# Kernel tuning notes

Hardware: AMD Instinct MI355X
Metric: run time of the kernel (lower is better)

## Reference

```python
import jax, jax.numpy as jnp
import numpy as np

NUM_EMBEDDINGS = 1024
EMBEDDING_DIM = 64


def setup_inputs() -> dict:
    key = jax.random.key(0)
    k1, k2 = jax.random.split(key)
    x = jax.random.normal(k1, (32, 64, 32, 32), dtype=jnp.float32)
    # embeddings initialized uniform(-1/K, 1/K) as in the torch module
    codebook = jax.random.uniform(
        k2, (NUM_EMBEDDINGS, EMBEDDING_DIM), dtype=jnp.float32,
        minval=-1.0 / NUM_EMBEDDINGS, maxval=1.0 / NUM_EMBEDDINGS)
    return {"x": x, "codebook": codebook}


def reference(x, codebook):
    # x: [B, D, H, W] -> [B, H, W, D]
    xp = jnp.transpose(x, (0, 2, 3, 1))
    B, H, W, D = xp.shape
    K = codebook.shape[0]
    xf = xp.reshape(-1, D)  # [N, D]
    # squared L2 distances via expansion (argmin identical to torch.norm argmin)
    x2 = jnp.sum(xf * xf, axis=1, keepdims=True)          # [N, 1]
    c2 = jnp.sum(codebook * codebook, axis=1)             # [K]
    d2 = x2 - 2.0 * (xf @ codebook.T) + c2[None, :]       # [N, K]
    idx = jnp.argmin(d2, axis=1)                          # [N]
    encodings = jax.nn.one_hot(idx, K, dtype=jnp.float32)  # [N, K]
    quantized = codebook[idx]                             # [N, D] == encodings @ codebook
    quantized = quantized.reshape(B, H, W, D).transpose(0, 3, 1, 2)
    return encodings, quantized
```

## Files before the change

### kernel.cpp

```cpp
#include <hip/hip_runtime.h>

#define N_PIX   32768
#define DIM     64
#define K_CODES 1024
#define NCHUNK  8
#define CHUNK   (K_CODES / NCHUNK)


__global__ __launch_bounds__(256) void c2_kernel(const float* __restrict__ cb,
                                                 float* __restrict__ c2) {
    int k = blockIdx.x * 256 + threadIdx.x;
    if (k >= K_CODES) return;
    const float* row = cb + k * DIM;
    float a0 = 0.f, a1 = 0.f, a2 = 0.f, a3 = 0.f;
#pragma unroll
    for (int d = 0; d < DIM; d += 4) {
        a0 = fmaf(row[d + 0], row[d + 0], a0);
        a1 = fmaf(row[d + 1], row[d + 1], a1);
        a2 = fmaf(row[d + 2], row[d + 2], a2);
        a3 = fmaf(row[d + 3], row[d + 3], a3);
    }
    c2[k] = (a0 + a1) + (a2 + a3);
}

__global__ __launch_bounds__(256) void argmin_partial(const float* __restrict__ x,
                                                      const float* __restrict__ cb,
                                                      const float* __restrict__ c2,
                                                      float2* __restrict__ part) {
    int blk    = blockIdx.x;
    int pixblk = blk >> 3;
    int chunk  = blk & 7;
    int p  = pixblk * 256 + threadIdx.x;
    int bb = p >> 10;
    int hw = p & 1023;

    const float* xbase = x + (size_t)bb * (DIM * 1024) + hw;
    float xv[DIM];
#pragma unroll
    for (int d = 0; d < DIM; ++d) xv[d] = xbase[(size_t)d * 1024];

    float s0 = 0.f, s1 = 0.f, s2 = 0.f, s3 = 0.f;
#pragma unroll
    for (int d = 0; d < DIM; d += 4) {
        s0 = fmaf(xv[d + 0], xv[d + 0], s0);
        s1 = fmaf(xv[d + 1], xv[d + 1], s1);
        s2 = fmaf(xv[d + 2], xv[d + 2], s2);
        s3 = fmaf(xv[d + 3], xv[d + 3], s3);
    }
    float x2 = (s0 + s1) + (s2 + s3);

    float best = 1e30f;
    int   bidx = 0;
    int   k0   = chunk * CHUNK;
#pragma unroll 2
    for (int k = k0; k < k0 + CHUNK; ++k) {
        const float* crow = cb + k * DIM;
        float a0 = 0.f, a1 = 0.f, a2 = 0.f, a3 = 0.f;
#pragma unroll
        for (int d = 0; d < DIM; d += 4) {
            a0 = fmaf(xv[d + 0], crow[d + 0], a0);
            a1 = fmaf(xv[d + 1], crow[d + 1], a1);
            a2 = fmaf(xv[d + 2], crow[d + 2], a2);
            a3 = fmaf(xv[d + 3], crow[d + 3], a3);
        }
        float dot = (a0 + a1) + (a2 + a3);
        float t    = x2 - 2.0f * dot;
        float dist = t + c2[k];
        if (dist < best) { best = dist; bidx = k; }
    }
    float2 r;
    r.x = best;
    r.y = __int_as_float(bidx);
    part[(size_t)chunk * N_PIX + p] = r;
}

__global__ __launch_bounds__(256) void finalize(const float* __restrict__ cb,
                                                const float2* __restrict__ part,
                                                float* __restrict__ enc,
                                                float* __restrict__ quant) {
    __shared__ int sidx[32];
    int block = blockIdx.x;
    int t     = threadIdx.x;

    if (t < 32) {
        int   n    = block * 32 + t;
        float best = 1e30f;
        int   bidx = 0;
#pragma unroll
        for (int c = 0; c < NCHUNK; ++c) {
            float2 r = part[(size_t)c * N_PIX + n];
            if (r.x < best) { best = r.x; bidx = __float_as_int(r.y); }
        }
        sidx[t] = bidx;
    }
    __syncthreads();

    int j0 = t * 4;
#pragma unroll 4
    for (int r = 0; r < 32; ++r) {
        int    n  = block * 32 + r;
        int    ir = sidx[r];
        float4 v;
        v.x = (ir == j0 + 0) ? 1.0f : 0.0f;
        v.y = (ir == j0 + 1) ? 1.0f : 0.0f;
        v.z = (ir == j0 + 2) ? 1.0f : 0.0f;
        v.w = (ir == j0 + 3) ? 1.0f : 0.0f;
        *reinterpret_cast<float4*>(enc + (size_t)n * K_CODES + j0) = v;
    }

    int r  = t & 31;
    int d0 = (t >> 5) * 8;
    int n  = block * 32 + r;
    int bb = n >> 10;
    int hw = n & 1023;
    int ir = sidx[r];
#pragma unroll
    for (int dd = 0; dd < 8; ++dd) {
        int d = d0 + dd;
        quant[(size_t)bb * (DIM * 1024) + (size_t)d * 1024 + hw] = cb[ir * DIM + d];
    }
}

extern "C" void kernel_launch(void* const* d_in, const int* in_sizes, int n_in,
                              void* d_out, int out_size, void* d_ws, size_t ws_size,
                              hipStream_t stream) {
    const float* x  = (const float*)d_in[0];
    const float* cb = (const float*)d_in[1];

    float*  c2   = (float*)d_ws;
    float2* part = (float2*)((char*)d_ws + 4096);

    float* enc   = (float*)d_out;
    float* quant = (float*)d_out + (size_t)N_PIX * K_CODES;

    c2_kernel<<<K_CODES / 256, 256, 0, stream>>>(cb, c2);
    argmin_partial<<<(N_PIX / 256) * NCHUNK, 256, 0, stream>>>(x, cb, c2, part);
    finalize<<<N_PIX / 32, 256, 0, stream>>>(cb, part, enc, quant);
}
```

Measured before the change: 250.4 us.

## Compute two pixels per thread in argmin and split finalize into reduce and one-hot kernels

The argmin kernel now has each thread handle two pixels, so every codebook value loaded is reused for two dot products. This halves the scalar codebook loads per FMA, at the cost of about twice the registers (launch bounds of 256,2). The finalize step is split into a per-pixel reduce plus quantized-output kernel, which stages indices in workspace, and a separate grid-stride kernel that writes the one-hot encodings. This adds a launch but gives each kernel simpler, more regular store patterns.

```diff
diff --git a/kernel.cpp b/kernel.cpp
--- a/kernel.cpp
+++ b/kernel.cpp
@@ -23,101 +23,122 @@
     c2[k] = (a0 + a1) + (a2 + a3);
 }
 
-__global__ __launch_bounds__(256) void argmin_partial(const float* __restrict__ x,
-                                                      const float* __restrict__ cb,
-                                                      const float* __restrict__ c2,
-                                                      float2* __restrict__ part) {
+__global__ __launch_bounds__(256, 2) void argmin_p2(const float* __restrict__ x,
+                                                    const float* __restrict__ cb,
+                                                    const float* __restrict__ c2,
+                                                    float2* __restrict__ part) {
     int blk    = blockIdx.x;
     int pixblk = blk >> 3;
     int chunk  = blk & 7;
-    int p  = pixblk * 256 + threadIdx.x;
-    int bb = p >> 10;
-    int hw = p & 1023;
+    int p0 = pixblk * 512 + threadIdx.x;
+    int bb = p0 >> 10;
+    int hw = p0 & 1023;
 
-    const float* xbase = x + (size_t)bb * (DIM * 1024) + hw;
-    float xv[DIM];
+    const float* xb0 = x + (size_t)bb * (DIM * 1024) + hw;
+    const float* xb1 = xb0 + 256;
+    float xv0[DIM], xv1[DIM];
 #pragma unroll
-    for (int d = 0; d < DIM; ++d) xv[d] = xbase[(size_t)d * 1024];
+    for (int d = 0; d < DIM; ++d) {
+        xv0[d] = xb0[(size_t)d << 10];
+        xv1[d] = xb1[(size_t)d << 10];
+    }
 
     float s0 = 0.f, s1 = 0.f, s2 = 0.f, s3 = 0.f;
+    float t0 = 0.f, t1 = 0.f, t2 = 0.f, t3 = 0.f;
 #pragma unroll
     for (int d = 0; d < DIM; d += 4) {
-        s0 = fmaf(xv[d + 0], xv[d + 0], s0);
-        s1 = fmaf(xv[d + 1], xv[d + 1], s1);
-        s2 = fmaf(xv[d + 2], xv[d + 2], s2);
-        s3 = fmaf(xv[d + 3], xv[d + 3], s3);
+        s0 = fmaf(xv0[d + 0], xv0[d + 0], s0);
+        s1 = fmaf(xv0[d + 1], xv0[d + 1], s1);
+        s2 = fmaf(xv0[d + 2], xv0[d + 2], s2);
+        s3 = fmaf(xv0[d + 3], xv0[d + 3], s3);
+        t0 = fmaf(xv1[d + 0], xv1[d + 0], t0);
+        t1 = fmaf(xv1[d + 1], xv1[d + 1], t1);
+        t2 = fmaf(xv1[d + 2], xv1[d + 2], t2);
+        t3 = fmaf(xv1[d + 3], xv1[d + 3], t3);
     }
-    float x2 = (s0 + s1) + (s2 + s3);
+    float x20 = (s0 + s1) + (s2 + s3);
+    float x21 = (t0 + t1) + (t2 + t3);
 
-    float best = 1e30f;
-    int   bidx = 0;
-    int   k0   = chunk * CHUNK;
+    float best0 = 1e30f, best1 = 1e30f;
+    int   bi0 = 0, bi1 = 0;
+    int   k0 = chunk * CHUNK;
 #pragma unroll 2
     for (int k = k0; k < k0 + CHUNK; ++k) {
         const float* crow = cb + k * DIM;
+        float c2k = c2[k];
         float a0 = 0.f, a1 = 0.f, a2 = 0.f, a3 = 0.f;
+        float b0 = 0.f, b1 = 0.f, b2 = 0.f, b3 = 0.f;
 #pragma unroll
         for (int d = 0; d < DIM; d += 4) {
-            a0 = fmaf(xv[d + 0], crow[d + 0], a0);
-            a1 = fmaf(xv[d + 1], crow[d + 1], a1);
-            a2 = fmaf(xv[d + 2], crow[d + 2], a2);
-            a3 = fmaf(xv[d + 3], crow[d + 3], a3);
+            float w0 = crow[d + 0], w1 = crow[d + 1];
+            float w2 = crow[d + 2], w3 = crow[d + 3];
+            a0 = fmaf(xv0[d + 0], w0, a0);
+            a1 = fmaf(xv0[d + 1], w1, a1);
+            a2 = fmaf(xv0[d + 2], w2, a2);
+            a3 = fmaf(xv0[d + 3], w3, a3);
+            b0 = fmaf(xv1[d + 0], w0, b0);
+            b1 = fmaf(xv1[d + 1], w1, b1);
+            b2 = fmaf(xv1[d + 2], w2, b2);
+            b3 = fmaf(xv1[d + 3], w3, b3);
         }
-        float dot = (a0 + a1) + (a2 + a3);
-        float t    = x2 - 2.0f * dot;
-        float dist = t + c2[k];
-        if (dist < best) { best = dist; bidx = k; }
+        float dot0 = (a0 + a1) + (a2 + a3);
+        float dot1 = (b0 + b1) + (b2 + b3);
+        float u0 = x20 - 2.0f * dot0;
+        float u1 = x21 - 2.0f * dot1;
+        float d0 = u0 + c2k;
+        float d1 = u1 + c2k;
+        if (d0 < best0) { best0 = d0; bi0 = k; }
+        if (d1 < best1) { best1 = d1; bi1 = k; }
     }
-    float2 r;
-    r.x = best;
-    r.y = __int_as_float(bidx);
-    part[(size_t)chunk * N_PIX + p] = r;
+    float2 r0; r0.x = best0; r0.y = __int_as_float(bi0);
+    float2 r1; r1.x = best1; r1.y = __int_as_float(bi1);
+    part[(size_t)chunk * N_PIX + p0]       = r0;
+    part[(size_t)chunk * N_PIX + p0 + 256] = r1;
 }
 
-__global__ __launch_bounds__(256) void finalize(const float* __restrict__ cb,
-                                                const float2* __restrict__ part,
-                                                float* __restrict__ enc,
-                                                float* __restrict__ quant) {
-    __shared__ int sidx[32];
-    int block = blockIdx.x;
-    int t     = threadIdx.x;
+__global__ __launch_bounds__(128) void reduce_quant(const float* __restrict__ cb,
+                                                    const float2* __restrict__ part,
+                                                    int* __restrict__ idx,
+                                                    float* __restrict__ quant) {
+    int n = blockIdx.x * 128 + threadIdx.x;
+    float best = 1e30f;
+    int   bi = 0;
+#pragma unroll
+    for (int c = 0; c < NCHUNK; ++c) {
+        float2 r = part[(size_t)c * N_PIX + n];
+        if (r.x < best) { best = r.x; bi = __float_as_int(r.y); }
+    }
+    idx[n] = bi;
 
-    if (t < 32) {
-        int   n    = block * 32 + t;
-        float best = 1e30f;
-        int   bidx = 0;
+    int bb = n >> 10;
+    int hw = n & 1023;
+    const float4* crow = reinterpret_cast<const float4*>(cb + (size_t)bi * DIM);
+    float* qb = quant + (size_t)bb * (DIM * 1024) + hw;
 #pragma unroll
-        for (int c = 0; c < NCHUNK; ++c) {
-            float2 r = part[(size_t)c * N_PIX + n];
-            if (r.x < best) { best = r.x; bidx = __float_as_int(r.y); }
-        }
-        sidx[t] = bidx;
+    for (int dq = 0; dq < 16; ++dq) {
+        float4 cv = crow[dq];
+        qb[(size_t)(dq * 4 + 0) << 10] = cv.x;
+        qb[(size_t)(dq * 4 + 1) << 10] = cv.y;
+        qb[(size_t)(dq * 4 + 2) << 10] = cv.z;
+        qb[(size_t)(dq * 4 + 3) << 10] = cv.w;
     }
-    __syncthreads();
+}
 
-    int j0 = t * 4;
-#pragma unroll 4
-    for (int r = 0; r < 32; ++r) {
-        int    n  = block * 32 + r;
-        int    ir = sidx[r];
+__global__ __launch_bounds__(256) void enc_write(const int* __restrict__ idx,
+                                                 float* __restrict__ enc) {
+    const int TOT = (N_PIX / 4) * K_CODES;
+    int tid = blockIdx.x * 256 + threadIdx.x;
+    float4* enc4 = reinterpret_cast<float4*>(enc);
+    for (int e = tid; e < TOT; e += 2048 * 256) {
+        int n  = e >> 8;
+        int j0 = (e & 255) << 2;
+        int ir = idx[n];
         float4 v;
         v.x = (ir == j0 + 0) ? 1.0f : 0.0f;
         v.y = (ir == j0 + 1) ? 1.0f : 0.0f;
         v.z = (ir == j0 + 2) ? 1.0f : 0.0f;
         v.w = (ir == j0 + 3) ? 1.0f : 0.0f;
-        *reinterpret_cast<float4*>(enc + (size_t)n * K_CODES + j0) = v;
-    }
-
-    int r  = t & 31;
-    int d0 = (t >> 5) * 8;
-    int n  = block * 32 + r;
-    int bb = n >> 10;
-    int hw = n & 1023;
-    int ir = sidx[r];
-#pragma unroll
-    for (int dd = 0; dd < 8; ++dd) {
-        int d = d0 + dd;
-        quant[(size_t)bb * (DIM * 1024) + (size_t)d * 1024 + hw] = cb[ir * DIM + d];
+        enc4[e] = v;
     }
 }
 
@@ -129,11 +150,13 @@
 
     float*  c2   = (float*)d_ws;
     float2* part = (float2*)((char*)d_ws + 4096);
+    int*    idx  = (int*)((char*)d_ws + 4096 + (size_t)NCHUNK * N_PIX * 8);
 
     float* enc   = (float*)d_out;
     float* quant = (float*)d_out + (size_t)N_PIX * K_CODES;
 
     c2_kernel<<<K_CODES / 256, 256, 0, stream>>>(cb, c2);
-    argmin_partial<<<(N_PIX / 256) * NCHUNK, 256, 0, stream>>>(x, cb, c2, part);
-    finalize<<<N_PIX / 32, 256, 0, stream>>>(cb, part, enc, quant);
+    argmin_p2<<<(N_PIX / 512) * NCHUNK, 256, 0, stream>>>(x, cb, c2, part);
+    reduce_quant<<<N_PIX / 128, 128, 0, stream>>>(cb, part, idx, quant);
+    enc_write<<<2048, 256, 0, stream>>>(idx, enc);
 }
```

After: 230.5 us. 1.09x faster.

## Stage codebook chunk in LDS and split finalize into reduce and one-hot kernels

Applied to the files above, without the earlier changes.

The argmin kernel now copies its 128-code slice of the codebook and the matching squared norms into shared memory, then reads them as float4 from LDS instead of reading global memory per code. The finalize step is split in two. One kernel reduces the partial results per pixel, writes the index to workspace and scatters the quantized vector. A grid-stride kernel then writes the one-hot matrix as float4. This aims to cut global-memory traffic in the distance loop and keep the large one-hot write fully coalesced, at the cost of an extra launch, an index round trip through memory, and 32KB of LDS per block, which may limit occupancy.

```diff
diff --git a/kernel.cpp b/kernel.cpp
--- a/kernel.cpp
+++ b/kernel.cpp
@@ -23,21 +23,36 @@
     c2[k] = (a0 + a1) + (a2 + a3);
 }
 
-__global__ __launch_bounds__(256) void argmin_partial(const float* __restrict__ x,
-                                                      const float* __restrict__ cb,
-                                                      const float* __restrict__ c2,
-                                                      float2* __restrict__ part) {
+__global__ __launch_bounds__(256, 4) void argmin_lds(const float* __restrict__ x,
+                                                     const float* __restrict__ cb,
+                                                     const float* __restrict__ c2,
+                                                     float2* __restrict__ part) {
+    __shared__ alignas(16) float lds_cb[CHUNK][DIM];
+    __shared__ float lds_c2[CHUNK];
+
     int blk    = blockIdx.x;
     int pixblk = blk >> 3;
     int chunk  = blk & 7;
-    int p  = pixblk * 256 + threadIdx.x;
+    int t  = threadIdx.x;
+    int k0 = chunk * CHUNK;
+
+    {
+        const float4* cb4  = reinterpret_cast<const float4*>(cb) + (size_t)k0 * (DIM / 4);
+        float4*       lds4 = reinterpret_cast<float4*>(&lds_cb[0][0]);
+#pragma unroll
+        for (int i = 0; i < (CHUNK * DIM / 4) / 256; ++i)
+            lds4[t + i * 256] = cb4[t + i * 256];
+        if (t < CHUNK) lds_c2[t] = c2[k0 + t];
+    }
+
+    int p  = pixblk * 256 + t;
     int bb = p >> 10;
     int hw = p & 1023;
 
     const float* xbase = x + (size_t)bb * (DIM * 1024) + hw;
     float xv[DIM];
 #pragma unroll
-    for (int d = 0; d < DIM; ++d) xv[d] = xbase[(size_t)d * 1024];
+    for (int d = 0; d < DIM; ++d) xv[d] = xbase[(size_t)d << 10];
 
     float s0 = 0.f, s1 = 0.f, s2 = 0.f, s3 = 0.f;
 #pragma unroll
@@ -49,23 +64,27 @@
     }
     float x2 = (s0 + s1) + (s2 + s3);
 
+    __syncthreads();
+
     float best = 1e30f;
     int   bidx = 0;
-    int   k0   = chunk * CHUNK;
 #pragma unroll 2
-    for (int k = k0; k < k0 + CHUNK; ++k) {
-        const float* crow = cb + k * DIM;
+    for (int kk = 0; kk < CHUNK; ++kk) {
+        const float* crow = &lds_cb[kk][0];
+        float c2k = lds_c2[kk];
         float a0 = 0.f, a1 = 0.f, a2 = 0.f, a3 = 0.f;
 #pragma unroll
         for (int d = 0; d < DIM; d += 4) {
-            a0 = fmaf(xv[d + 0], crow[d + 0], a0);
-            a1 = fmaf(xv[d + 1], crow[d + 1], a1);
-            a2 = fmaf(xv[d + 2], crow[d + 2], a2);
-            a3 = fmaf(xv[d + 3], crow[d + 3], a3);
+            float4 w = *reinterpret_cast<const float4*>(crow + d);
+            a0 = fmaf(xv[d + 0], w.x, a0);
+            a1 = fmaf(xv[d + 1], w.y, a1);
+            a2 = fmaf(xv[d + 2], w.z, a2);
+            a3 = fmaf(xv[d + 3], w.w, a3);
         }
         float dot = (a0 + a1) + (a2 + a3);
-        float t    = x2 - 2.0f * dot;
-        float dist = t + c2[k];
+        float u    = x2 - 2.0f * dot;
+        float dist = u + c2k;
+        int   k    = k0 + kk;
         if (dist < best) { best = dist; bidx = k; }
     }
     float2 r;
@@ -74,50 +93,49 @@
     part[(size_t)chunk * N_PIX + p] = r;
 }
 
-__global__ __launch_bounds__(256) void finalize(const float* __restrict__ cb,
-                                                const float2* __restrict__ part,
-                                                float* __restrict__ enc,
-                                                float* __restrict__ quant) {
-    __shared__ int sidx[32];
-    int block = blockIdx.x;
-    int t     = threadIdx.x;
+__global__ __launch_bounds__(128) void reduce_quant(const float* __restrict__ cb,
+                                                    const float2* __restrict__ part,
+                                                    int* __restrict__ idx,
+                                                    float* __restrict__ quant) {
+    int n = blockIdx.x * 128 + threadIdx.x;
+    float best = 1e30f;
+    int   bi = 0;
+#pragma unroll
+    for (int c = 0; c < NCHUNK; ++c) {
+        float2 r = part[(size_t)c * N_PIX + n];
+        if (r.x < best) { best = r.x; bi = __float_as_int(r.y); }
+    }
+    idx[n] = bi;
 
-    if (t < 32) {
-        int   n    = block * 32 + t;
-        float best = 1e30f;
-        int   bidx = 0;
+    int bb = n >> 10;
+    int hw = n & 1023;
+    const float4* crow = reinterpret_cast<const float4*>(cb + (size_t)bi * DIM);
+    float* qb = quant + (size_t)bb * (DIM * 1024) + hw;
 #pragma unroll
-        for (int c = 0; c < NCHUNK; ++c) {
-            float2 r = part[(size_t)c * N_PIX + n];
-            if (r.x < best) { best = r.x; bidx = __float_as_int(r.y); }
-        }
-        sidx[t] = bidx;
+    for (int dq = 0; dq < 16; ++dq) {
+        float4 cv = crow[dq];
+        qb[(size_t)(dq * 4 + 0) << 10] = cv.x;
+        qb[(size_t)(dq * 4 + 1) << 10] = cv.y;
+        qb[(size_t)(dq * 4 + 2) << 10] = cv.z;
+        qb[(size_t)(dq * 4 + 3) << 10] = cv.w;
     }
-    __syncthreads();
+}
 
-    int j0 = t * 4;
-#pragma unroll 4
-    for (int r = 0; r < 32; ++r) {
-        int    n  = block * 32 + r;
-        int    ir = sidx[r];
+__global__ __launch_bounds__(256) void enc_write(const int* __restrict__ idx,
+                                                 float* __restrict__ enc) {
+    const int TOT = (N_PIX / 4) * K_CODES;
+    int tid = blockIdx.x * 256 + threadIdx.x;
+    float4* enc4 = reinterpret_cast<float4*>(enc);
+    for (int e = tid; e < TOT; e += 2048 * 256) {
+        int n  = e >> 8;
+        int j0 = (e & 255) << 2;
+        int ir = idx[n];
         float4 v;
         v.x = (ir == j0 + 0) ? 1.0f : 0.0f;
         v.y = (ir == j0 + 1) ? 1.0f : 0.0f;
         v.z = (ir == j0 + 2) ? 1.0f : 0.0f;
         v.w = (ir == j0 + 3) ? 1.0f : 0.0f;
-        *reinterpret_cast<float4*>(enc + (size_t)n * K_CODES + j0) = v;
-    }
-
-    int r  = t & 31;
-    int d0 = (t >> 5) * 8;
-    int n  = block * 32 + r;
-    int bb = n >> 10;
-    int hw = n & 1023;
-    int ir = sidx[r];
-#pragma unroll
-    for (int dd = 0; dd < 8; ++dd) {
-        int d = d0 + dd;
-        quant[(size_t)bb * (DIM * 1024) + (size_t)d * 1024 + hw] = cb[ir * DIM + d];
+        enc4[e] = v;
     }
 }
 
@@ -129,11 +147,13 @@
 
     float*  c2   = (float*)d_ws;
     float2* part = (float2*)((char*)d_ws + 4096);
+    int*    idx  = (int*)((char*)d_ws + 4096 + (size_t)NCHUNK * N_PIX * 8);
 
     float* enc   = (float*)d_out;
     float* quant = (float*)d_out + (size_t)N_PIX * K_CODES;
 
     c2_kernel<<<K_CODES / 256, 256, 0, stream>>>(cb, c2);
-    argmin_partial<<<(N_PIX / 256) * NCHUNK, 256, 0, stream>>>(x, cb, c2, part);
-    finalize<<<N_PIX / 32, 256, 0, stream>>>(cb, part, enc, quant);
+    argmin_lds<<<(N_PIX / 256) * NCHUNK, 256, 0, stream>>>(x, cb, c2, part);
+    reduce_quant<<<N_PIX / 128, 128, 0, stream>>>(cb, part, idx, quant);
+    enc_write<<<2048, 256, 0, stream>>>(idx, enc);
 }
```

Measured after the change: 255.0 us. About the same (+1.8%).
